# Optimization experiments

Measured on AMD Instinct MI355X. Metric: run time of the kernel, lower is better.

## Reference

```python
import jax, jax.numpy as jnp
import numpy as np

N_NODES = 50000
N_EDGES = 800000
NODE_DIM = 10
EDGE_DIM = 5
HID = 64


def _tconv(x, src, dst, e_attr, wq, bq, wk, bk, wv, bv, we, ws, bs):
    # PyG TransformerConv, heads=1, concat=True, root_weight=True, beta=False
    n = x.shape[0]
    q = x @ wq + bq                      # [N, HID]
    k = x @ wk + bk                      # [N, HID]
    v = x @ wv + bv                      # [N, HID]
    ee = e_attr @ we                     # [E, HID] (lin_edge, no bias)
    ke = k[src] + ee                     # key per edge
    ve = v[src] + ee                     # value per edge
    logits = jnp.sum(q[dst] * ke, axis=-1) / 8.0  # sqrt(64) = 8
    m = jax.ops.segment_max(logits, dst, num_segments=n)
    p = jnp.exp(logits - m[dst])
    s = jax.ops.segment_sum(p, dst, num_segments=n)
    alpha = p / s[dst]                   # segment softmax over in-neighbors
    agg = jax.ops.segment_sum(alpha[:, None] * ve, dst, num_segments=n)
    return agg + x @ ws + bs             # + lin_skip(x_i)


def setup_inputs() -> dict:
    key = jax.random.key(0)
    ks = jax.random.split(key, 32)
    x = jax.random.uniform(ks[0], (N_NODES, NODE_DIM), dtype=jnp.float32)
    edge_index = jax.random.randint(ks[1], (2, N_EDGES), 0, N_NODES, dtype=jnp.int64)
    edge_attr = jax.random.uniform(ks[2], (N_EDGES, EDGE_DIM), dtype=jnp.float32)

    def lin(k, fan_in, fan_out):
        b = 1.0 / np.sqrt(fan_in)
        return jax.random.uniform(k, (fan_in, fan_out), jnp.float32, -b, b)

    def bias(k, fan_in, fan_out):
        b = 1.0 / np.sqrt(fan_in)
        return jax.random.uniform(k, (fan_out,), jnp.float32, -b, b)

    inp = dict(x=x, edge_index=edge_index, edge_attr=edge_attr)
    # conv1: NODE_DIM -> HID
    inp['w1q'] = lin(ks[3], NODE_DIM, HID); inp['b1q'] = bias(ks[4], NODE_DIM, HID)
    inp['w1k'] = lin(ks[5], NODE_DIM, HID); inp['b1k'] = bias(ks[6], NODE_DIM, HID)
    inp['w1v'] = lin(ks[7], NODE_DIM, HID); inp['b1v'] = bias(ks[8], NODE_DIM, HID)
    inp['w1e'] = lin(ks[9], EDGE_DIM, HID)
    inp['w1s'] = lin(ks[10], NODE_DIM, HID); inp['b1s'] = bias(ks[11], NODE_DIM, HID)
    # 5 stacked HID -> HID layers
    inp['wq'] = jnp.stack([lin(jax.random.fold_in(ks[12], i), HID, HID) for i in range(5)])
    inp['bq'] = jnp.stack([bias(jax.random.fold_in(ks[13], i), HID, HID) for i in range(5)])
    inp['wk'] = jnp.stack([lin(jax.random.fold_in(ks[14], i), HID, HID) for i in range(5)])
    inp['bk'] = jnp.stack([bias(jax.random.fold_in(ks[15], i), HID, HID) for i in range(5)])
    inp['wv'] = jnp.stack([lin(jax.random.fold_in(ks[16], i), HID, HID) for i in range(5)])
    inp['bv'] = jnp.stack([bias(jax.random.fold_in(ks[17], i), HID, HID) for i in range(5)])
    inp['we'] = jnp.stack([lin(jax.random.fold_in(ks[18], i), EDGE_DIM, HID) for i in range(5)])
    inp['ws'] = jnp.stack([lin(jax.random.fold_in(ks[19], i), HID, HID) for i in range(5)])
    inp['bs'] = jnp.stack([bias(jax.random.fold_in(ks[20], i), HID, HID) for i in range(5)])
    # final linear HID -> 1
    inp['lin_w'] = lin(ks[21], HID, 1); inp['lin_b'] = bias(ks[22], HID, 1)
    return inp


def reference(x, edge_index, edge_attr, w1q, b1q, w1k, b1k, w1v, b1v, w1e, w1s, b1s,
              wq, bq, wk, bk, wv, bv, we, ws, bs, lin_w, lin_b):
    src, dst = edge_index[0], edge_index[1]  # x_j = x[src], aggregated into dst
    h = jnp.log(x + 1.0)
    e = jnp.log(edge_attr + 1.0)
    h = _tconv(h, src, dst, e, w1q, b1q, w1k, b1k, w1v, b1v, w1e, w1s, b1s)
    for i in range(5):
        h = _tconv(h, src, dst, e, wq[i], bq[i], wk[i], bk[i], wv[i], bv[i], we[i], ws[i], bs[i])
    return h @ lin_w + lin_b  # [N, 1]
```

## Files before the change

### kernel.cpp

```cpp
#include <hip/hip_runtime.h>
#include <hip/hip_fp16.h>
#include <cstdint>
#include <cstddef>

#define NN 50000
#define NE 800000
#define HD 64
#define SB 49

__global__ void k_hist(const int* __restrict__ ei, int* __restrict__ cnt) {
    int e = blockIdx.x * blockDim.x + threadIdx.x;
    if (e < NE) atomicAdd(&cnt[ei[NE + e]], 1);
}

__global__ __launch_bounds__(256) void k_scan1(const int* __restrict__ cnt,
                                               int* __restrict__ row_start,
                                               int* __restrict__ bsum) {
    __shared__ int ssum[256];
    const int tid = threadIdx.x, b = blockIdx.x;
    const int i0 = b * 1024 + tid * 4;
    int c0 = 0, c1 = 0, c2 = 0, c3 = 0;
    if (i0 + 3 < NN) {
        const int4 c = *(const int4*)(cnt + i0);
        c0 = c.x; c1 = c.y; c2 = c.z; c3 = c.w;
    } else {
        if (i0 + 0 < NN) c0 = cnt[i0 + 0];
        if (i0 + 1 < NN) c1 = cnt[i0 + 1];
        if (i0 + 2 < NN) c2 = cnt[i0 + 2];
        if (i0 + 3 < NN) c3 = cnt[i0 + 3];
    }
    ssum[tid] = c0 + c1 + c2 + c3;
    __syncthreads();
    for (int off = 1; off < 256; off <<= 1) {
        int v = (tid >= off) ? ssum[tid - off] : 0;
        __syncthreads();
        ssum[tid] += v;
        __syncthreads();
    }
    int ex = (tid == 0) ? 0 : ssum[tid - 1];
    if (i0 + 0 < NN) row_start[i0 + 0] = ex;
    ex += c0;
    if (i0 + 1 < NN) row_start[i0 + 1] = ex;
    ex += c1;
    if (i0 + 2 < NN) row_start[i0 + 2] = ex;
    ex += c2;
    if (i0 + 3 < NN) row_start[i0 + 3] = ex;
    if (tid == 255) bsum[b] = ssum[255];
}

__global__ __launch_bounds__(64) void k_scan2(const int* __restrict__ bsum,
                                              int* __restrict__ boff,
                                              int* __restrict__ row_start) {
    __shared__ int s[64];
    const int t = threadIdx.x;
    s[t] = (t < SB) ? bsum[t] : 0;
    __syncthreads();
    for (int off = 1; off < 64; off <<= 1) {
        int v = (t >= off) ? s[t - off] : 0;
        __syncthreads();
        s[t] += v;
        __syncthreads();
    }
    if (t < SB) boff[t] = (t == 0) ? 0 : s[t - 1];
    if (t == 0) row_start[NN] = s[SB - 1];
}

__global__ __launch_bounds__(256) void k_scan3(int* __restrict__ row_start,
                                               const int* __restrict__ boff,
                                               int* __restrict__ cur) {
    const int b = blockIdx.x;
    const int i0 = b * 1024 + threadIdx.x * 4;
    const int o = boff[b];
#pragma unroll
    for (int k = 0; k < 4; ++k) {
        int i = i0 + k;
        if (i < NN) {
            int v = row_start[i] + o;
            row_start[i] = v;
            cur[i] = v;
        }
    }
}

__global__ void k_scatter(const int* __restrict__ ei, const float* __restrict__ ea,
                          int* __restrict__ cur, float* __restrict__ e5lo,
                          float* __restrict__ e5hi) {
    int e = blockIdx.x * blockDim.x + threadIdx.x;
    if (e < NE) {
        int d = ei[NE + e];
        int pos = atomicAdd(&cur[d], 1);
        float4 lo;
        lo.x = __logf(ea[e * 5 + 0] + 1.f);
        lo.y = __logf(ea[e * 5 + 1] + 1.f);
        lo.z = __logf(ea[e * 5 + 2] + 1.f);
        lo.w = __logf(ea[e * 5 + 3] + 1.f);
        float2 hi;
        hi.x = __logf(ea[e * 5 + 4] + 1.f);
        hi.y = __int_as_float(ei[e] << 8);
        *(float4*)(e5lo + (size_t)pos * 4) = lo;
        *(float2*)(e5hi + (size_t)pos * 2) = hi;
    }
}

__device__ __forceinline__ void cvt_kv(const uint4 u, float4& k4, float4& v4) {
    const float2 p0 = __half22float2(*(const __half2*)&u.x);
    const float2 p1 = __half22float2(*(const __half2*)&u.y);
    const float2 p2 = __half22float2(*(const __half2*)&u.z);
    const float2 p3 = __half22float2(*(const __half2*)&u.w);
    k4 = make_float4(p0.x, p1.x, p2.x, p3.x);
    v4 = make_float4(p0.y, p1.y, p2.y, p3.y);
}

__global__ __launch_bounds__(256) void k_qkvs64(
    const float* __restrict__ h,
    const float* __restrict__ Wq, const float* __restrict__ Bq,
    const float* __restrict__ Wk, const float* __restrict__ Bk,
    const float* __restrict__ Wv, const float* __restrict__ Bv,
    const float* __restrict__ Ws, const float* __restrict__ Bs,
    float* __restrict__ qb, __half* __restrict__ kvh, float* __restrict__ sb) {
    __shared__ float xs[4][256];
    const int lane = threadIdx.x & 63;
    const int w = threadIdx.x >> 6;
    const int pair = w >> 1, half = w & 1;
    const float* W0 = half ? Wk : Wq;
    const float* B0 = half ? Bk : Bq;
    const float* W1 = half ? Wv : Ws;
    const float* B1 = half ? Bv : Bs;
    const float scl0 = half ? 1.f : 0.125f;
    float w0[64], w1[64];
#pragma unroll
    for (int j = 0; j < 64; ++j) {
        w0[j] = W0[j * 64 + lane] * scl0;
        w1[j] = W1[j * 64 + lane];
    }
    const float b0 = B0[lane] * scl0, b1 = B1[lane];
    const int nquad = NN / 4;
    const int step = gridDim.x * 2;
    int quad = blockIdx.x * 2 + pair;
    if (quad >= nquad) return;
    {
        const float4 g = *(const float4*)(h + (size_t)quad * 256 + lane * 4);
        *(float4*)&xs[w][lane * 4] = g;
    }
    while (true) {
        const int nq = quad + step;
        const bool more = nq < nquad;
        float4 gn;
        if (more) gn = *(const float4*)(h + (size_t)nq * 256 + lane * 4);
        float a0[4] = {b0, b0, b0, b0};
        float a1[4] = {b1, b1, b1, b1};
#pragma unroll
        for (int jq = 0; jq < 16; ++jq) {
#pragma unroll
            for (int n = 0; n < 4; ++n) {
                const float4 xv = *(const float4*)&xs[w][n * 64 + jq * 4];
                a0[n] = fmaf(xv.x, w0[jq * 4 + 0], a0[n]);
                a1[n] = fmaf(xv.x, w1[jq * 4 + 0], a1[n]);
                a0[n] = fmaf(xv.y, w0[jq * 4 + 1], a0[n]);
                a1[n] = fmaf(xv.y, w1[jq * 4 + 1], a1[n]);
                a0[n] = fmaf(xv.z, w0[jq * 4 + 2], a0[n]);
                a1[n] = fmaf(xv.z, w1[jq * 4 + 2], a1[n]);
                a0[n] = fmaf(xv.w, w0[jq * 4 + 3], a0[n]);
                a1[n] = fmaf(xv.w, w1[jq * 4 + 3], a1[n]);
            }
        }
#pragma unroll
        for (int n = 0; n < 4; ++n) {
            const size_t node = (size_t)(quad * 4 + n);
            if (half == 0) {
                qb[node * 64 + lane] = a0[n];
                sb[node * 64 + lane] = a1[n];
            } else {
                const __half2 hv = __floats2half2_rn(a0[n], a1[n]);
                *(__half2*)(kvh + node * 128 + lane * 2) = hv;
            }
        }
        if (!more) break;
        *(float4*)&xs[w][lane * 4] = gn;
        quad = nq;
    }
}

__global__ __launch_bounds__(256, 4) void k_qkvs10(
    const float* __restrict__ x,
    const float* __restrict__ Wq, const float* __restrict__ Bq,
    const float* __restrict__ Wk, const float* __restrict__ Bk,
    const float* __restrict__ Wv, const float* __restrict__ Bv,
    const float* __restrict__ Ws, const float* __restrict__ Bs,
    float* __restrict__ qb, __half* __restrict__ kvh, float* __restrict__ sb) {
    __shared__ float xs[640];
    const int lane = threadIdx.x & 63;
    const int w = threadIdx.x >> 6;
    const bool iskv = (w == 1 || w == 3);
    const float* WA = (w == 0) ? Wq : iskv ? Wk : Ws;
    const float* BA = (w == 0) ? Bq : iskv ? Bk : Bs;
    const float scl = (w == 0) ? 0.125f : 1.f;
    float wrA[10], wrB[10];
#pragma unroll
    for (int j = 0; j < 10; ++j) {
        wrA[j] = WA[j * 64 + lane] * scl;
        wrB[j] = iskv ? Wv[j * 64 + lane] : 0.f;
    }
    const float bA = BA[lane] * scl;
    const float bB = iskv ? Bv[lane] : 0.f;
    const int tile = blockIdx.x;
    const int fbase = tile * 640;
    const int fcnt = min(640, NN * 10 - fbase);
    if (threadIdx.x * 4 < fcnt) {
        float4 v = *(const float4*)(x + (size_t)fbase + threadIdx.x * 4);
        v.x = __logf(v.x + 1.f);
        v.y = __logf(v.y + 1.f);
        v.z = __logf(v.z + 1.f);
        v.w = __logf(v.w + 1.f);
        *(float4*)&xs[threadIdx.x * 4] = v;
    }
    __syncthreads();
    const int nbase = tile * 64;
    const int nodes = min(64, NN - nbase);
    const int n0 = (w == 3) ? 32 : 0;
    const int n1 = iskv ? ((w == 1) ? min(nodes, 32) : nodes) : nodes;
    for (int n = n0; n < n1; ++n) {
        float accA = bA, accB = bB;
#pragma unroll
        for (int j = 0; j < 10; ++j) {
            const float xv = xs[n * 10 + j];
            accA = fmaf(xv, wrA[j], accA);
            accB = fmaf(xv, wrB[j], accB);
        }
        const size_t node = (size_t)(nbase + n);
        if (iskv) {
            const __half2 hv = __floats2half2_rn(accA, accB);
            *(__half2*)(kvh + node * 128 + lane * 2) = hv;
        } else if (w == 0) {
            qb[node * 64 + lane] = accA;
        } else {
            sb[node * 64 + lane] = accA;
        }
    }
}

template <bool FINAL>
__global__ __launch_bounds__(256) void k_agg(
    const float* __restrict__ q, const __half* __restrict__ kv,
    const float* __restrict__ sk, const float* __restrict__ e5lo,
    const float* __restrict__ e5hi, const float* __restrict__ wE,
    const int* __restrict__ row_start, float* __restrict__ hout,
    const float* __restrict__ lw, const float* lb) {
    const int lane = threadIdx.x & 63;
    const int g = lane >> 4, t = lane & 15;
    const int node = __builtin_amdgcn_readfirstlane(blockIdx.x * 4 + (threadIdx.x >> 6));
    if (node >= NN) return;
    const int beg = row_start[node], end = row_start[node + 1];
    if (beg == end) {
        const float4 s4 = *(const float4*)(sk + (size_t)node * 64 + t * 4);
        if (FINAL) {
            const float4 lw4 = *(const float4*)(lw + t * 4);
            float r = s4.x * lw4.x;
            r = fmaf(s4.y, lw4.y, r);
            r = fmaf(s4.z, lw4.z, r);
            r = fmaf(s4.w, lw4.w, r);
            r += __shfl_xor(r, 1);
            r += __shfl_xor(r, 2);
            r += __shfl_xor(r, 4);
            r += __shfl_xor(r, 8);
            if (lane == 0) hout[node] = r + lb[0];
        } else if (g == 0) {
            *(float4*)(hout + (size_t)node * 64 + t * 4) = s4;
        }
        return;
    }
    const float4 q4 = *(const float4*)(q + (size_t)node * 64 + t * 4);
    float g5[5];
    {
        const float4 wg = *(const float4*)(wE + g * 64 + t * 4);
        float dc = q4.x * wg.x;
        dc = fmaf(q4.y, wg.y, dc);
        dc = fmaf(q4.z, wg.z, dc);
        dc = fmaf(q4.w, wg.w, dc);
        dc += __shfl_xor(dc, 1);
        dc += __shfl_xor(dc, 2);
        dc += __shfl_xor(dc, 4);
        dc += __shfl_xor(dc, 8);
        const float4 w4 = *(const float4*)(wE + 4 * 64 + t * 4);
        float d4 = q4.x * w4.x;
        d4 = fmaf(q4.y, w4.y, d4);
        d4 = fmaf(q4.z, w4.z, d4);
        d4 = fmaf(q4.w, w4.w, d4);
        d4 += __shfl_xor(d4, 1);
        d4 += __shfl_xor(d4, 2);
        d4 += __shfl_xor(d4, 4);
        d4 += __shfl_xor(d4, 8);
        g5[0] = __shfl(dc, 0);
        g5[1] = __shfl(dc, 16);
        g5[2] = __shfl(dc, 32);
        g5[3] = __shfl(dc, 48);
        g5[4] = __shfl(d4, 0);
    }
    float m = -1e30f, l = 0.f;
    float4 accv = {0.f, 0.f, 0.f, 0.f};
    float a50 = 0.f, a51 = 0.f, a52 = 0.f, a53 = 0.f, a54 = 0.f;
    const char* kvc = (const char*)kv;
    const int i0x = beg + g;
    const int i0 = (i0x < end) ? i0x : beg;
    float4 e0lo = *(const float4*)(e5lo + (size_t)i0 * 4);
    float2 e0hi = *(const float2*)(e5hi + (size_t)i0 * 2);
    const int i1x = beg + 4 + g;
    const int i1 = (i1x < end) ? i1x : beg;
    float4 e1lo = *(const float4*)(e5lo + (size_t)i1 * 4);
    float2 e1hi = *(const float2*)(e5hi + (size_t)i1 * 2);
    uint4 kv8 = *(const uint4*)(kvc + (size_t)(unsigned)__float_as_int(e0hi.y) + t * 16);
#pragma unroll 2
    for (int p = beg; p < end; p += 4) {
        const int nx = p + 8 + g;
        const int npp = (nx < end) ? nx : beg;
        const float4 nlo = *(const float4*)(e5lo + (size_t)npp * 4);
        const float2 nhi = *(const float2*)(e5hi + (size_t)npp * 2);
        const uint4 nkv =
            *(const uint4*)(kvc + (size_t)(unsigned)__float_as_int(e1hi.y) + t * 16);
        const bool act = (p + g) < end;
        float4 k4, v4;
        cvt_kv(kv8, k4, v4);
        float d = q4.x * k4.x;
        d = fmaf(q4.y, k4.y, d);
        d = fmaf(q4.z, k4.z, d);
        d = fmaf(q4.w, k4.w, d);
        d += __shfl_xor(d, 1);
        d += __shfl_xor(d, 2);
        d += __shfl_xor(d, 4);
        d += __shfl_xor(d, 8);
        float d5 = g5[0] * e0lo.x;
        d5 = fmaf(g5[1], e0lo.y, d5);
        d5 = fmaf(g5[2], e0lo.z, d5);
        d5 = fmaf(g5[3], e0lo.w, d5);
        d5 = fmaf(g5[4], e0hi.x, d5);
        const float la = act ? (d + d5) : -1e30f;
        const float nm = fmaxf(m, la);
        const float scl = __expf(m - nm);
        const float pa = __expf(la - nm);
        l = fmaf(l, scl, pa);
        accv.x = fmaf(accv.x, scl, pa * v4.x);
        accv.y = fmaf(accv.y, scl, pa * v4.y);
        accv.z = fmaf(accv.z, scl, pa * v4.z);
        accv.w = fmaf(accv.w, scl, pa * v4.w);
        a50 = fmaf(a50, scl, pa * e0lo.x);
        a51 = fmaf(a51, scl, pa * e0lo.y);
        a52 = fmaf(a52, scl, pa * e0lo.z);
        a53 = fmaf(a53, scl, pa * e0lo.w);
        a54 = fmaf(a54, scl, pa * e0hi.x);
        m = nm;
        e0lo = e1lo;
        e0hi = e1hi;
        e1lo = nlo;
        e1hi = nhi;
        kv8 = nkv;
    }
    float M = fmaxf(m, __shfl_xor(m, 16));
    M = fmaxf(M, __shfl_xor(M, 32));
    const float f = __expf(m - M);
    float lz = l * f;
    lz += __shfl_xor(lz, 16);
    lz += __shfl_xor(lz, 32);
    accv.x *= f;
    accv.y *= f;
    accv.z *= f;
    accv.w *= f;
    a50 *= f;
    a51 *= f;
    a52 *= f;
    a53 *= f;
    a54 *= f;
#pragma unroll
    for (int s = 16; s <= 32; s <<= 1) {
        accv.x += __shfl_xor(accv.x, s);
        accv.y += __shfl_xor(accv.y, s);
        accv.z += __shfl_xor(accv.z, s);
        accv.w += __shfl_xor(accv.w, s);
        a50 += __shfl_xor(a50, s);
        a51 += __shfl_xor(a51, s);
        a52 += __shfl_xor(a52, s);
        a53 += __shfl_xor(a53, s);
        a54 += __shfl_xor(a54, s);
    }
    float4 t4 = accv;
    {
        const float4 w0 = *(const float4*)(wE + 0 * 64 + t * 4);
        const float4 w1 = *(const float4*)(wE + 1 * 64 + t * 4);
        const float4 w2 = *(const float4*)(wE + 2 * 64 + t * 4);
        const float4 w3 = *(const float4*)(wE + 3 * 64 + t * 4);
        const float4 w4r = *(const float4*)(wE + 4 * 64 + t * 4);
        t4.x = fmaf(a50, w0.x, t4.x);
        t4.y = fmaf(a50, w0.y, t4.y);
        t4.z = fmaf(a50, w0.z, t4.z);
        t4.w = fmaf(a50, w0.w, t4.w);
        t4.x = fmaf(a51, w1.x, t4.x);
        t4.y = fmaf(a51, w1.y, t4.y);
        t4.z = fmaf(a51, w1.z, t4.z);
        t4.w = fmaf(a51, w1.w, t4.w);
        t4.x = fmaf(a52, w2.x, t4.x);
        t4.y = fmaf(a52, w2.y, t4.y);
        t4.z = fmaf(a52, w2.z, t4.z);
        t4.w = fmaf(a52, w2.w, t4.w);
        t4.x = fmaf(a53, w3.x, t4.x);
        t4.y = fmaf(a53, w3.y, t4.y);
        t4.z = fmaf(a53, w3.z, t4.z);
        t4.w = fmaf(a53, w3.w, t4.w);
        t4.x = fmaf(a54, w4r.x, t4.x);
        t4.y = fmaf(a54, w4r.y, t4.y);
        t4.z = fmaf(a54, w4r.z, t4.z);
        t4.w = fmaf(a54, w4r.w, t4.w);
    }
    const float4 s4 = *(const float4*)(sk + (size_t)node * 64 + t * 4);
    const float rl = 1.f / lz;
    float4 o;
    o.x = fmaf(t4.x, rl, s4.x);
    o.y = fmaf(t4.y, rl, s4.y);
    o.z = fmaf(t4.z, rl, s4.z);
    o.w = fmaf(t4.w, rl, s4.w);
    if (FINAL) {
        const float4 lw4 = *(const float4*)(lw + t * 4);
        float r = o.x * lw4.x;
        r = fmaf(o.y, lw4.y, r);
        r = fmaf(o.z, lw4.z, r);
        r = fmaf(o.w, lw4.w, r);
        r += __shfl_xor(r, 1);
        r += __shfl_xor(r, 2);
        r += __shfl_xor(r, 4);
        r += __shfl_xor(r, 8);
        if (lane == 0) hout[node] = r + lb[0];
    } else if (g == 0) {
        *(float4*)(hout + (size_t)node * 64 + t * 4) = o;
    }
}

extern "C" void kernel_launch(void* const* d_in, const int* in_sizes, int n_in,
                              void* d_out, int out_size, void* d_ws, size_t ws_size,
                              hipStream_t stream) {
    const float* x = (const float*)d_in[0];
    const int* ei = (const int*)d_in[1];
    const float* ea = (const float*)d_in[2];
    const float* w1q = (const float*)d_in[3];
    const float* b1q = (const float*)d_in[4];
    const float* w1k = (const float*)d_in[5];
    const float* b1k = (const float*)d_in[6];
    const float* w1v = (const float*)d_in[7];
    const float* b1v = (const float*)d_in[8];
    const float* w1e = (const float*)d_in[9];
    const float* w1s = (const float*)d_in[10];
    const float* b1s = (const float*)d_in[11];
    const float* wq = (const float*)d_in[12];
    const float* bq = (const float*)d_in[13];
    const float* wk = (const float*)d_in[14];
    const float* bk = (const float*)d_in[15];
    const float* wv = (const float*)d_in[16];
    const float* bv = (const float*)d_in[17];
    const float* we = (const float*)d_in[18];
    const float* ws = (const float*)d_in[19];
    const float* bs = (const float*)d_in[20];
    const float* lw = (const float*)d_in[21];
    const float* lb = (const float*)d_in[22];

    uintptr_t p = (uintptr_t)d_ws;
    auto alloc = [&](size_t bytes) -> void* {
        void* r = (void*)p;
        p += (bytes + 255) & ~(size_t)255;
        return r;
    };
    float* e5lo = (float*)alloc((size_t)NE * 4 * 4);
    float* e5hi = (float*)alloc((size_t)NE * 2 * 4);
    float* hb = (float*)alloc((size_t)NN * HD * 4);
    __half* kvh = (__half*)alloc((size_t)NN * 128 * 2);
    float* qb = (float*)alloc((size_t)NN * HD * 4);
    float* sb = (float*)alloc((size_t)NN * HD * 4);
    int* row_start = (int*)alloc((size_t)(NN + 1) * 4);
    int* cnt = (int*)alloc((size_t)NN * 4);
    int* cur = (int*)alloc((size_t)NN * 4);
    int* bsum = (int*)alloc((size_t)SB * 4);
    int* boff = (int*)alloc((size_t)SB * 4);

    hipMemsetAsync(cnt, 0, (size_t)NN * 4, stream);
    k_hist<<<(NE + 255) / 256, 256, 0, stream>>>(ei, cnt);
    k_scan1<<<SB, 256, 0, stream>>>(cnt, row_start, bsum);
    k_scan2<<<1, 64, 0, stream>>>(bsum, boff, row_start);
    k_scan3<<<SB, 256, 0, stream>>>(row_start, boff, cur);
    k_scatter<<<(NE + 255) / 256, 256, 0, stream>>>(ei, ea, cur, e5lo, e5hi);

    const int gg64 = 512;
    const int gg10 = (NN + 63) / 64;
    const int agg_grid = (NN + 3) / 4;

    k_qkvs10<<<gg10, 256, 0, stream>>>(x, w1q, b1q, w1k, b1k, w1v, b1v, w1s, b1s,
                                       qb, kvh, sb);
    k_agg<false><<<agg_grid, 256, 0, stream>>>(qb, kvh, sb, e5lo, e5hi, w1e,
                                               row_start, hb, lw, lb);

    for (int i = 0; i < 5; ++i) {
        k_qkvs64<<<gg64, 256, 0, stream>>>(hb, wq + i * 4096, bq + i * 64,
                                           wk + i * 4096, bk + i * 64,
                                           wv + i * 4096, bv + i * 64,
                                           ws + i * 4096, bs + i * 64,
                                           qb, kvh, sb);
        if (i < 4) {
            k_agg<false><<<agg_grid, 256, 0, stream>>>(qb, kvh, sb, e5lo, e5hi,
                                                       we + i * 320, row_start, hb,
                                                       lw, lb);
        } else {
            k_agg<true><<<agg_grid, 256, 0, stream>>>(qb, kvh, sb, e5lo, e5hi,
                                                      we + i * 320, row_start,
                                                      (float*)d_out, lw, lb);
        }
    }
}
```

Before: 742.8 us.

## Pack edge records into 16-byte half-precision structs and restructure QKVS GEMM

Edge attributes and source offsets are packed into one 16-byte record per edge: five log-transformed attributes in fp16 plus the source index in the upper 16 bits. This replaces separate 16-byte and 8-byte float arrays, so the aggregation loop issues one load per edge instead of two. Separately, the 64-wide QKVS kernel now gives each wave a single weight matrix (64 registers instead of 128) and processes 8-node tiles with a shared-memory double buffer and block syncs, with K passed through LDS to pair with V. The changes lower register pressure and edge bandwidth, but fp16 attributes cost precision and the source index in 16 bits only holds if the kv byte offset, index times 256, fits in 24 bits; 50000 nodes exceeds 65535? No, 50000 fits, but the packing is fragile.

```diff
diff --git a/kernel.cpp b/kernel.cpp
--- a/kernel.cpp
+++ b/kernel.cpp
@@ -7,6 +7,7 @@
 #define NE 800000
 #define HD 64
 #define SB 49
+#define NT64 6250
 
 __global__ void k_hist(const int* __restrict__ ei, int* __restrict__ cnt) {
     int e = blockIdx.x * blockDim.x + threadIdx.x;
@@ -83,22 +84,26 @@
 }
 
 __global__ void k_scatter(const int* __restrict__ ei, const float* __restrict__ ea,
-                          int* __restrict__ cur, float* __restrict__ e5lo,
-                          float* __restrict__ e5hi) {
+                          int* __restrict__ cur, uint4* __restrict__ e5p) {
     int e = blockIdx.x * blockDim.x + threadIdx.x;
     if (e < NE) {
         int d = ei[NE + e];
         int pos = atomicAdd(&cur[d], 1);
-        float4 lo;
-        lo.x = __logf(ea[e * 5 + 0] + 1.f);
-        lo.y = __logf(ea[e * 5 + 1] + 1.f);
-        lo.z = __logf(ea[e * 5 + 2] + 1.f);
-        lo.w = __logf(ea[e * 5 + 3] + 1.f);
-        float2 hi;
-        hi.x = __logf(ea[e * 5 + 4] + 1.f);
-        hi.y = __int_as_float(ei[e] << 8);
-        *(float4*)(e5lo + (size_t)pos * 4) = lo;
-        *(float2*)(e5hi + (size_t)pos * 2) = hi;
+        const float e0 = __logf(ea[e * 5 + 0] + 1.f);
+        const float e1 = __logf(ea[e * 5 + 1] + 1.f);
+        const float e2 = __logf(ea[e * 5 + 2] + 1.f);
+        const float e3 = __logf(ea[e * 5 + 3] + 1.f);
+        const float e4 = __logf(ea[e * 5 + 4] + 1.f);
+        union { __half2 h; unsigned u; } c01, c23;
+        c01.h = __floats2half2_rn(e0, e1);
+        c23.h = __floats2half2_rn(e2, e3);
+        uint4 rec;
+        rec.x = c01.u;
+        rec.y = c23.u;
+        rec.z = ((unsigned)ei[e] << 16) |
+                (unsigned)__half_as_ushort(__float2half_rn(e4));
+        rec.w = 0u;
+        e5p[pos] = rec;
     }
 }
 
@@ -111,73 +116,74 @@
     v4 = make_float4(p0.y, p1.y, p2.y, p3.y);
 }
 
-__global__ __launch_bounds__(256) void k_qkvs64(
+__global__ __launch_bounds__(256, 4) void k_qkvs64(
     const float* __restrict__ h,
     const float* __restrict__ Wq, const float* __restrict__ Bq,
     const float* __restrict__ Wk, const float* __restrict__ Bk,
     const float* __restrict__ Wv, const float* __restrict__ Bv,
     const float* __restrict__ Ws, const float* __restrict__ Bs,
     float* __restrict__ qb, __half* __restrict__ kvh, float* __restrict__ sb) {
-    __shared__ float xs[4][256];
+    __shared__ float xs[2][512];
+    __shared__ float kls[512];
     const int lane = threadIdx.x & 63;
     const int w = threadIdx.x >> 6;
-    const int pair = w >> 1, half = w & 1;
-    const float* W0 = half ? Wk : Wq;
-    const float* B0 = half ? Bk : Bq;
-    const float* W1 = half ? Wv : Ws;
-    const float* B1 = half ? Bv : Bs;
-    const float scl0 = half ? 1.f : 0.125f;
-    float w0[64], w1[64];
-#pragma unroll
-    for (int j = 0; j < 64; ++j) {
-        w0[j] = W0[j * 64 + lane] * scl0;
-        w1[j] = W1[j * 64 + lane];
-    }
-    const float b0 = B0[lane] * scl0, b1 = B1[lane];
-    const int nquad = NN / 4;
-    const int step = gridDim.x * 2;
-    int quad = blockIdx.x * 2 + pair;
-    if (quad >= nquad) return;
+    const float* W = (w == 0) ? Wq : (w == 1) ? Ws : (w == 2) ? Wk : Wv;
+    const float* B = (w == 0) ? Bq : (w == 1) ? Bs : (w == 2) ? Bk : Bv;
+    const float scl = (w == 0) ? 0.125f : 1.f;
+    float wr[64];
+#pragma unroll
+    for (int j = 0; j < 64; ++j) wr[j] = W[j * 64 + lane] * scl;
+    const float bias = B[lane] * scl;
+
+    int tile = blockIdx.x;
     {
-        const float4 g = *(const float4*)(h + (size_t)quad * 256 + lane * 4);
-        *(float4*)&xs[w][lane * 4] = g;
-    }
+        const float2 g = *(const float2*)(h + (size_t)tile * 512 + threadIdx.x * 2);
+        *(float2*)&xs[0][threadIdx.x * 2] = g;
+    }
+    __syncthreads();
+    int buf = 0;
     while (true) {
-        const int nq = quad + step;
-        const bool more = nq < nquad;
-        float4 gn;
-        if (more) gn = *(const float4*)(h + (size_t)nq * 256 + lane * 4);
-        float a0[4] = {b0, b0, b0, b0};
-        float a1[4] = {b1, b1, b1, b1};
+        const int nt = tile + gridDim.x;
+        const bool more = nt < NT64;
+        float2 gn;
+        if (more) gn = *(const float2*)(h + (size_t)nt * 512 + threadIdx.x * 2);
+        float acc[8] = {bias, bias, bias, bias, bias, bias, bias, bias};
 #pragma unroll
         for (int jq = 0; jq < 16; ++jq) {
 #pragma unroll
-            for (int n = 0; n < 4; ++n) {
-                const float4 xv = *(const float4*)&xs[w][n * 64 + jq * 4];
-                a0[n] = fmaf(xv.x, w0[jq * 4 + 0], a0[n]);
-                a1[n] = fmaf(xv.x, w1[jq * 4 + 0], a1[n]);
-                a0[n] = fmaf(xv.y, w0[jq * 4 + 1], a0[n]);
-                a1[n] = fmaf(xv.y, w1[jq * 4 + 1], a1[n]);
-                a0[n] = fmaf(xv.z, w0[jq * 4 + 2], a0[n]);
-                a1[n] = fmaf(xv.z, w1[jq * 4 + 2], a1[n]);
-                a0[n] = fmaf(xv.w, w0[jq * 4 + 3], a0[n]);
-                a1[n] = fmaf(xv.w, w1[jq * 4 + 3], a1[n]);
+            for (int n = 0; n < 8; ++n) {
+                const float4 xv = *(const float4*)&xs[buf][n * 64 + jq * 4];
+                acc[n] = fmaf(xv.x, wr[jq * 4 + 0], acc[n]);
+                acc[n] = fmaf(xv.y, wr[jq * 4 + 1], acc[n]);
+                acc[n] = fmaf(xv.z, wr[jq * 4 + 2], acc[n]);
+                acc[n] = fmaf(xv.w, wr[jq * 4 + 3], acc[n]);
             }
         }
-#pragma unroll
-        for (int n = 0; n < 4; ++n) {
-            const size_t node = (size_t)(quad * 4 + n);
-            if (half == 0) {
-                qb[node * 64 + lane] = a0[n];
-                sb[node * 64 + lane] = a1[n];
-            } else {
-                const __half2 hv = __floats2half2_rn(a0[n], a1[n]);
-                *(__half2*)(kvh + node * 128 + lane * 2) = hv;
+        if (w == 2) {
+#pragma unroll
+            for (int n = 0; n < 8; ++n) kls[n * 64 + lane] = acc[n];
+        }
+        if (more) *(float2*)&xs[buf ^ 1][threadIdx.x * 2] = gn;
+        __syncthreads();
+        const int nb = tile * 8;
+        if (w == 0) {
+#pragma unroll
+            for (int n = 0; n < 8; ++n) qb[(size_t)(nb + n) * 64 + lane] = acc[n];
+        } else if (w == 1) {
+#pragma unroll
+            for (int n = 0; n < 8; ++n) sb[(size_t)(nb + n) * 64 + lane] = acc[n];
+        } else if (w == 3) {
+#pragma unroll
+            for (int n = 0; n < 8; ++n) {
+                const float kk = kls[n * 64 + lane];
+                *(__half2*)(kvh + (size_t)(nb + n) * 128 + lane * 2) =
+                    __floats2half2_rn(kk, acc[n]);
             }
         }
         if (!more) break;
-        *(float4*)&xs[w][lane * 4] = gn;
-        quad = nq;
+        __syncthreads();
+        tile = nt;
+        buf ^= 1;
     }
 }
 
@@ -242,10 +248,9 @@
 template <bool FINAL>
 __global__ __launch_bounds__(256) void k_agg(
     const float* __restrict__ q, const __half* __restrict__ kv,
-    const float* __restrict__ sk, const float* __restrict__ e5lo,
-    const float* __restrict__ e5hi, const float* __restrict__ wE,
-    const int* __restrict__ row_start, float* __restrict__ hout,
-    const float* __restrict__ lw, const float* lb) {
+    const float* __restrict__ sk, const uint4* __restrict__ e5p,
+    const float* __restrict__ wE, const int* __restrict__ row_start,
+    float* __restrict__ hout, const float* __restrict__ lw, const float* lb) {
     const int lane = threadIdx.x & 63;
     const int g = lane >> 4, t = lane & 15;
     const int node = __builtin_amdgcn_readfirstlane(blockIdx.x * 4 + (threadIdx.x >> 6));
@@ -302,24 +307,26 @@
     const char* kvc = (const char*)kv;
     const int i0x = beg + g;
     const int i0 = (i0x < end) ? i0x : beg;
-    float4 e0lo = *(const float4*)(e5lo + (size_t)i0 * 4);
-    float2 e0hi = *(const float2*)(e5hi + (size_t)i0 * 2);
+    uint4 r0 = e5p[i0];
     const int i1x = beg + 4 + g;
     const int i1 = (i1x < end) ? i1x : beg;
-    float4 e1lo = *(const float4*)(e5lo + (size_t)i1 * 4);
-    float2 e1hi = *(const float2*)(e5hi + (size_t)i1 * 2);
-    uint4 kv8 = *(const uint4*)(kvc + (size_t)(unsigned)__float_as_int(e0hi.y) + t * 16);
+    uint4 r1 = e5p[i1];
+    uint4 kv8 =
+        *(const uint4*)(kvc + (size_t)((r0.z & 0xffff0000u) >> 8) + t * 16);
 #pragma unroll 2
     for (int p = beg; p < end; p += 4) {
         const int nx = p + 8 + g;
         const int npp = (nx < end) ? nx : beg;
-        const float4 nlo = *(const float4*)(e5lo + (size_t)npp * 4);
-        const float2 nhi = *(const float2*)(e5hi + (size_t)npp * 2);
+        const uint4 rn = e5p[npp];
         const uint4 nkv =
-            *(const uint4*)(kvc + (size_t)(unsigned)__float_as_int(e1hi.y) + t * 16);
+            *(const uint4*)(kvc + (size_t)((r1.z & 0xffff0000u) >> 8) + t * 16);
         const bool act = (p + g) < end;
         float4 k4, v4;
         cvt_kv(kv8, k4, v4);
+        const float2 e01 = __half22float2(*(const __half2*)&r0.x);
+        const float2 e23 = __half22float2(*(const __half2*)&r0.y);
+        const float e4v =
+            __half2float(__ushort_as_half((unsigned short)(r0.z & 0xffffu)));
         float d = q4.x * k4.x;
         d = fmaf(q4.y, k4.y, d);
         d = fmaf(q4.z, k4.z, d);
@@ -328,11 +335,11 @@
         d += __shfl_xor(d, 2);
         d += __shfl_xor(d, 4);
         d += __shfl_xor(d, 8);
-        float d5 = g5[0] * e0lo.x;
-        d5 = fmaf(g5[1], e0lo.y, d5);
-        d5 = fmaf(g5[2], e0lo.z, d5);
-        d5 = fmaf(g5[3], e0lo.w, d5);
-        d5 = fmaf(g5[4], e0hi.x, d5);
+        float d5 = g5[0] * e01.x;
+        d5 = fmaf(g5[1], e01.y, d5);
+        d5 = fmaf(g5[2], e23.x, d5);
+        d5 = fmaf(g5[3], e23.y, d5);
+        d5 = fmaf(g5[4], e4v, d5);
         const float la = act ? (d + d5) : -1e30f;
         const float nm = fmaxf(m, la);
         const float scl = __expf(m - nm);
@@ -342,16 +349,14 @@
         accv.y = fmaf(accv.y, scl, pa * v4.y);
         accv.z = fmaf(accv.z, scl, pa * v4.z);
         accv.w = fmaf(accv.w, scl, pa * v4.w);
-        a50 = fmaf(a50, scl, pa * e0lo.x);
-        a51 = fmaf(a51, scl, pa * e0lo.y);
-        a52 = fmaf(a52, scl, pa * e0lo.z);
-        a53 = fmaf(a53, scl, pa * e0lo.w);
-        a54 = fmaf(a54, scl, pa * e0hi.x);
+        a50 = fmaf(a50, scl, pa * e01.x);
+        a51 = fmaf(a51, scl, pa * e01.y);
+        a52 = fmaf(a52, scl, pa * e23.x);
+        a53 = fmaf(a53, scl, pa * e23.y);
+        a54 = fmaf(a54, scl, pa * e4v);
         m = nm;
-        e0lo = e1lo;
-        e0hi = e1hi;
-        e1lo = nlo;
-        e1hi = nhi;
+        r0 = r1;
+        r1 = rn;
         kv8 = nkv;
     }
     float M = fmaxf(m, __shfl_xor(m, 16));
@@ -465,8 +470,7 @@
         p += (bytes + 255) & ~(size_t)255;
         return r;
     };
-    float* e5lo = (float*)alloc((size_t)NE * 4 * 4);
-    float* e5hi = (float*)alloc((size_t)NE * 2 * 4);
+    uint4* e5p = (uint4*)alloc((size_t)NE * 16);
     float* hb = (float*)alloc((size_t)NN * HD * 4);
     __half* kvh = (__half*)alloc((size_t)NN * 128 * 2);
     float* qb = (float*)alloc((size_t)NN * HD * 4);
@@ -482,16 +486,16 @@
     k_scan1<<<SB, 256, 0, stream>>>(cnt, row_start, bsum);
     k_scan2<<<1, 64, 0, stream>>>(bsum, boff, row_start);
     k_scan3<<<SB, 256, 0, stream>>>(row_start, boff, cur);
-    k_scatter<<<(NE + 255) / 256, 256, 0, stream>>>(ei, ea, cur, e5lo, e5hi);
-
-    const int gg64 = 512;
+    k_scatter<<<(NE + 255) / 256, 256, 0, stream>>>(ei, ea, cur, e5p);
+
+    const int gg64 = 1024;
     const int gg10 = (NN + 63) / 64;
     const int agg_grid = (NN + 3) / 4;
 
     k_qkvs10<<<gg10, 256, 0, stream>>>(x, w1q, b1q, w1k, b1k, w1v, b1v, w1s, b1s,
                                        qb, kvh, sb);
-    k_agg<false><<<agg_grid, 256, 0, stream>>>(qb, kvh, sb, e5lo, e5hi, w1e,
-                                               row_start, hb, lw, lb);
+    k_agg<false><<<agg_grid, 256, 0, stream>>>(qb, kvh, sb, e5p, w1e, row_start,
+                                               hb, lw, lb);
 
     for (int i = 0; i < 5; ++i) {
         k_qkvs64<<<gg64, 256, 0, stream>>>(hb, wq + i * 4096, bq + i * 64,
@@ -500,11 +504,11 @@
                                            ws + i * 4096, bs + i * 64,
                                            qb, kvh, sb);
         if (i < 4) {
-            k_agg<false><<<agg_grid, 256, 0, stream>>>(qb, kvh, sb, e5lo, e5hi,
+            k_agg<false><<<agg_grid, 256, 0, stream>>>(qb, kvh, sb, e5p,
                                                        we + i * 320, row_start, hb,
                                                        lw, lb);
         } else {
-            k_agg<true><<<agg_grid, 256, 0, stream>>>(qb, kvh, sb, e5lo, e5hi,
+            k_agg<true><<<agg_grid, 256, 0, stream>>>(qb, kvh, sb, e5p,
                                                       we + i * 320, row_start,
                                                       (float*)d_out, lw, lb);
         }
```

Result: faster. 640.8 us (-13.7%).
